# Kernel tuning notes

Measured on AMD Instinct MI355X. Metric: run time of the kernel, lower is better.

The kernel has to match this reference:

```python
import jax, jax.numpy as jnp
import numpy as np
from jax import lax

B, S, D, NH, K = 4, 2048, 1024, 16, 3
EPS = 1e-6


def custom_layernorm(x, gamma, beta):
    # torch-style: std with ddof=1, eps added to std (not var)
    mean = jnp.mean(x, axis=-1, keepdims=True)
    var = jnp.sum((x - mean) ** 2, axis=-1, keepdims=True) / (x.shape[-1] - 1)
    std = jnp.sqrt(var)
    return gamma * ((x - mean) / (std + EPS)) + beta


def setup_inputs() -> dict:
    key = jax.random.key(0)
    ks = jax.random.split(key, 10)
    s = 1.0 / np.sqrt(D)
    return {
        "x": jax.random.normal(ks[0], (B, S, D), jnp.float32),
        "Wq": jax.random.normal(ks[1], (D, D), jnp.float32) * s,
        "bq": jax.random.normal(ks[2], (D,), jnp.float32) * 0.02,
        "Wk": jax.random.normal(ks[3], (D, D), jnp.float32) * s,
        "Wv": jax.random.normal(ks[4], (D, D), jnp.float32) * s,
        "bv": jax.random.normal(ks[5], (D,), jnp.float32) * 0.02,
        "conv_w": jax.random.normal(ks[6], (D, D // NH, K), jnp.float32) * (1.0 / np.sqrt((D // NH) * K)),
        "conv_b": jax.random.normal(ks[7], (D,), jnp.float32) * 0.02,
        "gamma": jnp.ones((D,), jnp.float32),
        "beta": jnp.zeros((D,), jnp.float32),
        "Wo": jax.random.normal(ks[8], (D, D), jnp.float32) * s,
        "bo": jax.random.normal(ks[9], (D,), jnp.float32) * 0.02,
    }


def reference(x, Wq, bq, Wk, Wv, bv, conv_w, conv_b, gamma, beta, Wo, bo):
    d = x.shape[-1]
    groups = d // conv_w.shape[1]
    pad = conv_w.shape[2] // 2

    q = x @ Wq + bq
    k = x @ Wk  # key has no bias
    v = x @ Wv + bv

    # grouped conv1d over sequence dim (NCW layout)
    xc = jnp.transpose(x, (0, 2, 1))  # [B, D, S]
    conv_out = lax.conv_general_dilated(
        xc, conv_w, window_strides=(1,), padding=[(pad, pad)],
        feature_group_count=groups,
        dimension_numbers=("NCH", "OIH", "NCH"),
    ) + conv_b[None, :, None]
    conv_out = jnp.transpose(conv_out, (0, 2, 1))  # [B, S, D]
    conv_out = custom_layernorm(conv_out, gamma, beta)  # dropout = identity (eval)

    scale = 1.0 / jnp.sqrt(jnp.asarray(d, x.dtype))
    scores = jnp.einsum("bqd,bkd->bqk", q, k) * scale  # [B, S, S]
    attn = jax.nn.softmax(scores, axis=-1)
    attention_out = jnp.einsum("bqk,bkd->bqd", attn, v)

    combined = custom_layernorm(conv_out + attention_out, gamma, beta)
    return combined @ Wo + bo + x
```

## Files before the change

kernel.cpp:

```cpp
#include <hip/hip_runtime.h>
#include <cstdint>


#define DEV __device__ __forceinline__

typedef unsigned short u16;
typedef __attribute__((ext_vector_type(8))) short bf16x8;
typedef __attribute__((ext_vector_type(4))) float f32x4;

static const int Sn = 2048, Dn = 1024;

DEV float bf2f(u16 u) { union { unsigned int i; float f; } w; w.i = ((unsigned int)u) << 16; return w.f; }
DEV u16 f2bf(float f) {
  union { float f; unsigned int i; } w; w.f = f;
  unsigned int x = w.i;
  return (u16)((x + 0x7FFFu + ((x >> 16) & 1u)) >> 16);
}

DEV void gload_lds16(const u16* gsrc, u16* lds_dst) {
  __builtin_amdgcn_global_load_lds(
      (const __attribute__((address_space(1))) void*)gsrc,
      (__attribute__((address_space(3))) void*)lds_dst,
      16, 0, 0);
}

DEV float block_allreduce_sum(float v, float* red, int tid) {
  #pragma unroll
  for (int o = 32; o > 0; o >>= 1) v += __shfl_down(v, o, 64);
  __syncthreads();
  if ((tid & 63) == 0) red[tid >> 6] = v;
  __syncthreads();
  return red[0] + red[1] + red[2] + red[3];
}

DEV float block_allreduce_max(float v, float* red, int tid) {
  #pragma unroll
  for (int o = 32; o > 0; o >>= 1) v = fmaxf(v, __shfl_down(v, o, 64));
  __syncthreads();
  if ((tid & 63) == 0) red[tid >> 6] = v;
  __syncthreads();
  return fmaxf(fmaxf(red[0], red[1]), fmaxf(red[2], red[3]));
}

__global__ __launch_bounds__(256)
void prep_all(const float* __restrict__ Wq, const float* __restrict__ Wk,
              const float* __restrict__ Wv, const float* __restrict__ Wo,
              u16* __restrict__ wT,
              const float* __restrict__ bq, const float* __restrict__ bv,
              float* __restrict__ qkvb,
              const float* __restrict__ cw, u16* __restrict__ wconv,
              const float* __restrict__ x, u16* __restrict__ xb) {
  __shared__ u16 sm[64][68];
  int blk = blockIdx.x;
  int tid = threadIdx.x;
  if (blk < 1024) {
    int w = blk >> 8, t = blk & 255;
    const float* src = (w == 0) ? Wq : (w == 1) ? Wk : (w == 2) ? Wv : Wo;
    u16* dst = wT + (size_t)w * 1048576u;
    int i0 = (t >> 4) << 6, j0 = (t & 15) << 6;
    int tx = tid & 15, r0 = tid >> 4;
    #pragma unroll
    for (int rr = r0; rr < 64; rr += 16) {
      float4 v = *(const float4*)&src[(long)(i0 + rr) * 1024 + j0 + tx * 4];
      sm[rr][tx*4+0] = f2bf(v.x); sm[rr][tx*4+1] = f2bf(v.y);
      sm[rr][tx*4+2] = f2bf(v.z); sm[rr][tx*4+3] = f2bf(v.w);
    }
    __syncthreads();
    #pragma unroll
    for (int cc = r0; cc < 64; cc += 16) {
      ushort4 o;
      o.x = sm[tx*4+0][cc]; o.y = sm[tx*4+1][cc];
      o.z = sm[tx*4+2][cc]; o.w = sm[tx*4+3][cc];
      *(ushort4*)&dst[(long)(j0 + cc) * 1024 + i0 + tx * 4] = o;
    }
  } else if (blk < 1040) {
    int oc0 = (blk - 1024) * 64;
    for (int idx = tid; idx < 64 * 192; idx += 256) {
      int oc = oc0 + idx / 192; int k = idx % 192;
      int t = k >> 6, i = k & 63;
      wconv[(long)oc * 192 + k] = f2bf(cw[(long)oc * 192 + i * 3 + t]);
    }
  } else if (blk == 1040) {
    for (int j = tid; j < 3072; j += 256) {
      float v = 0.0f;
      if (j < 1024) v = bq[j];
      else if (j >= 2048) v = bv[j - 2048];
      qkvb[j] = v;
    }
  } else {
    int i = (blk - 1041) * 1024 + tid * 4;
    float4 v = *(const float4*)&x[i];
    ushort4 o;
    o.x = f2bf(v.x); o.y = f2bf(v.y); o.z = f2bf(v.z); o.w = f2bf(v.w);
    *(ushort4*)&xb[i] = o;
  }
}

template<typename CT>
__global__ __launch_bounds__(256, 2)
void gemm_nt(const u16* __restrict__ A, const u16* __restrict__ A2, long Abs, int lda,
             const u16* __restrict__ B, long Bbs, int ldb,
             CT* __restrict__ C, CT* __restrict__ C2, long Cbs, int ldc,
             int zsplit, int K, float scale,
             const float* __restrict__ bias, int bias_bs,
             const float* __restrict__ res, long Rbs, int ldr) {
  __shared__ u16 sA[2][128 * 32];
  __shared__ u16 sB[2][128 * 32];
  int tid = threadIdx.x;
  int lane = tid & 63, wv = tid >> 6;
  int quad = lane >> 4, lm = lane & 15;
  int wr = wv >> 1, wc = wv & 1;
  long m0 = (long)blockIdx.x * 128, n0 = (long)blockIdx.y * 128;
  int z = blockIdx.z;
  if (z >= zsplit) { A = A2 + (long)(z - zsplit) * Abs; C = C2 + (long)(z - zsplit) * Cbs; }
  else             { A = A  + (long)z * Abs;            C = C  + (long)z * Cbs; }
  B += (long)z * Bbs;
  if (res) res += (long)z * Rbs;

  f32x4 acc[4][4] = {};

  int srow = wv * 16 + (lane >> 2);
  int sch = (lane & 3) * 8;
  const u16* Ap = A + (m0 + srow) * (long)lda + sch;
  const u16* Bp = B + (n0 + srow) * (long)ldb + sch;
  const int lofs = wv * 16 * 32;

  for (int k0 = 0; k0 < K; k0 += 64) {
    #pragma unroll
    for (int h = 0; h < 2; h++) {
      int kh = k0 + h * 32;
      gload_lds16(Ap + kh, &sA[h][lofs]);
      gload_lds16(Ap + 64 * (long)lda + kh, &sA[h][lofs + 64 * 32]);
      gload_lds16(Bp + kh, &sB[h][lofs]);
      gload_lds16(Bp + 64 * (long)ldb + kh, &sB[h][lofs + 64 * 32]);
    }
    __syncthreads();
    #pragma unroll
    for (int h = 0; h < 2; h++) {
      bf16x8 af[4], bfr[4];
      #pragma unroll
      for (int mi = 0; mi < 4; mi++)
        af[mi] = *(const bf16x8*)&sA[h][(wr * 64 + mi * 16 + lm) * 32 + quad * 8];
      #pragma unroll
      for (int ni = 0; ni < 4; ni++)
        bfr[ni] = *(const bf16x8*)&sB[h][(wc * 64 + ni * 16 + lm) * 32 + quad * 8];
      #pragma unroll
      for (int mi = 0; mi < 4; mi++)
        #pragma unroll
        for (int ni = 0; ni < 4; ni++)
          acc[mi][ni] = __builtin_amdgcn_mfma_f32_16x16x32_bf16(af[mi], bfr[ni], acc[mi][ni], 0, 0, 0);
    }
    __syncthreads();
  }

  #pragma unroll
  for (int mi = 0; mi < 4; mi++) {
    #pragma unroll
    for (int ni = 0; ni < 4; ni++) {
      int col = (int)n0 + wc * 64 + ni * 16 + lm;
      float bv = bias ? bias[(long)z * bias_bs + col] : 0.0f;
      #pragma unroll
      for (int r = 0; r < 4; r++) {
        long rowg = m0 + wr * 64 + mi * 16 + quad * 4 + r;
        float v = acc[mi][ni][r] * scale + bv;
        if (res) v += res[rowg * (long)ldr + col];
        if constexpr (sizeof(CT) == 2) C[rowg * (long)ldc + col] = f2bf(v);
        else                           C[rowg * (long)ldc + col] = v;
      }
    }
  }
}

__global__ __launch_bounds__(256)
void mid_all(const u16* __restrict__ xb, const u16* __restrict__ wt,
             const float* __restrict__ cb, u16* __restrict__ convo,
             const u16* __restrict__ Vb, u16* __restrict__ vt) {
  __shared__ u16 smem[9360];
  int blk = blockIdx.x;
  int tid = threadIdx.x;
  if (blk < 1024) {
    u16 (*sx)[72] = (u16(*)[72])smem;
    int s0 = (blk & 15) * 128;
    int g = (blk >> 4) & 15;
    int b = blk >> 8;
    int lane = tid & 63, wv = tid >> 6;
    int quad = lane >> 4, lm = lane & 15;
    for (int idx = tid; idx < 130 * 16; idx += 256) {
      int r = idx >> 4, c4 = (idx & 15) * 4;
      int s = s0 - 1 + r;
      ushort4 v;
      if (s >= 0 && s < Sn) v = *(const ushort4*)&xb[((long)b * Sn + s) * Dn + g * 64 + c4];
      else { v.x = 0; v.y = 0; v.z = 0; v.w = 0; }
      *(ushort4*)&sx[r][c4] = v;
    }
    __syncthreads();
    f32x4 acc[2][4] = {};
    const u16* wg = wt + (long)g * 64 * 192;
    #pragma unroll
    for (int ks = 0; ks < 6; ks++) {
      int t = ks >> 1;
      int i0 = (ks & 1) * 32 + quad * 8;
      bf16x8 a0 = *(const bf16x8*)&sx[wv * 32 + lm + t][i0];
      bf16x8 a1 = *(const bf16x8*)&sx[wv * 32 + 16 + lm + t][i0];
      #pragma unroll
      for (int nf = 0; nf < 4; nf++) {
        bf16x8 bf = *(const bf16x8*)&wg[(nf * 16 + lm) * 192 + ks * 32 + quad * 8];
        acc[0][nf] = __builtin_amdgcn_mfma_f32_16x16x32_bf16(a0, bf, acc[0][nf], 0, 0, 0);
        acc[1][nf] = __builtin_amdgcn_mfma_f32_16x16x32_bf16(a1, bf, acc[1][nf], 0, 0, 0);
      }
    }
    #pragma unroll
    for (int mi = 0; mi < 2; mi++) {
      #pragma unroll
      for (int nf = 0; nf < 4; nf++) {
        int col = g * 64 + nf * 16 + lm;
        float bias = cb[col];
        #pragma unroll
        for (int r = 0; r < 4; r++) {
          int row = wv * 32 + mi * 16 + quad * 4 + r;
          convo[((long)b * Sn + s0 + row) * Dn + col] = f2bf(acc[mi][nf][r] + bias);
        }
      }
    }
  } else {
    u16 (*sm)[68] = (u16(*)[68])smem;
    int t = blk - 1024;
    int b = t >> 9, r = t & 511;
    int j0 = (r & 15) << 6, i0 = ((r >> 4) & 31) << 6;
    const u16* s = Vb + (long)b * Sn * Dn;
    u16* d = vt + (long)b * Dn * Sn;
    int tx = tid & 15, r0 = tid >> 4;
    #pragma unroll
    for (int rr = r0; rr < 64; rr += 16) {
      ushort4 v = *(const ushort4*)&s[(long)(i0 + rr) * 1024 + j0 + tx * 4];
      sm[rr][tx*4+0] = v.x; sm[rr][tx*4+1] = v.y; sm[rr][tx*4+2] = v.z; sm[rr][tx*4+3] = v.w;
    }
    __syncthreads();
    #pragma unroll
    for (int cc = r0; cc < 64; cc += 16) {
      ushort4 o;
      o.x = sm[tx*4+0][cc]; o.y = sm[tx*4+1][cc];
      o.z = sm[tx*4+2][cc]; o.w = sm[tx*4+3][cc];
      *(ushort4*)&d[(long)(j0 + cc) * 2048 + i0 + tx * 4] = o;
    }
  }
}

__global__ __launch_bounds__(256)
void ln_kernel(const u16* __restrict__ a, const u16* __restrict__ b2,
               const float* __restrict__ gamma, const float* __restrict__ beta,
               u16* __restrict__ out) {
  __shared__ float red[4];
  long row = blockIdx.x;
  int tid = threadIdx.x;
  long base = row * Dn + tid * 4;
  ushort4 av = *(const ushort4*)&a[base];
  float v0 = bf2f(av.x), v1 = bf2f(av.y), v2 = bf2f(av.z), v3 = bf2f(av.w);
  if (b2) {
    ushort4 bv4 = *(const ushort4*)&b2[base];
    v0 += bf2f(bv4.x); v1 += bf2f(bv4.y); v2 += bf2f(bv4.z); v3 += bf2f(bv4.w);
  }
  float s = block_allreduce_sum(v0 + v1 + v2 + v3, red, tid);
  float mean = s * (1.0f / 1024.0f);
  float d0 = v0 - mean, d1 = v1 - mean, d2 = v2 - mean, d3 = v3 - mean;
  float sq = block_allreduce_sum(d0 * d0 + d1 * d1 + d2 * d2 + d3 * d3, red, tid);
  float inv = 1.0f / (sqrtf(sq * (1.0f / 1023.0f)) + 1e-6f);
  float4 gv = *(const float4*)&gamma[tid * 4];
  float4 bev = *(const float4*)&beta[tid * 4];
  ushort4 o;
  o.x = f2bf(gv.x * d0 * inv + bev.x);
  o.y = f2bf(gv.y * d1 * inv + bev.y);
  o.z = f2bf(gv.z * d2 * inv + bev.z);
  o.w = f2bf(gv.w * d3 * inv + bev.w);
  *(ushort4*)&out[base] = o;
}

__global__ __launch_bounds__(256)
void softmax_bf16(u16* __restrict__ pa, u16* __restrict__ pb, int rowsplit) {
  __shared__ float red[4];
  long row = blockIdx.x;
  u16* p = (row < rowsplit) ? pa + row * 2048 : pb + (row - rowsplit) * 2048;
  int tid = threadIdx.x;
  ushort4 a = *(const ushort4*)&p[tid * 8];
  ushort4 b = *(const ushort4*)&p[tid * 8 + 4];
  float f0 = bf2f(a.x), f1 = bf2f(a.y), f2 = bf2f(a.z), f3 = bf2f(a.w);
  float f4 = bf2f(b.x), f5 = bf2f(b.y), f6 = bf2f(b.z), f7 = bf2f(b.w);
  float m = fmaxf(fmaxf(fmaxf(f0, f1), fmaxf(f2, f3)),
                  fmaxf(fmaxf(f4, f5), fmaxf(f6, f7)));
  m = block_allreduce_max(m, red, tid);
  float e0 = __expf(f0 - m), e1 = __expf(f1 - m), e2 = __expf(f2 - m), e3 = __expf(f3 - m);
  float e4 = __expf(f4 - m), e5 = __expf(f5 - m), e6 = __expf(f6 - m), e7 = __expf(f7 - m);
  float s = block_allreduce_sum(e0 + e1 + e2 + e3 + e4 + e5 + e6 + e7, red, tid);
  float inv = 1.0f / s;
  ushort4 o1, o2;
  o1.x = f2bf(e0 * inv); o1.y = f2bf(e1 * inv); o1.z = f2bf(e2 * inv); o1.w = f2bf(e3 * inv);
  o2.x = f2bf(e4 * inv); o2.y = f2bf(e5 * inv); o2.z = f2bf(e6 * inv); o2.w = f2bf(e7 * inv);
  *(ushort4*)&p[tid * 8] = o1;
  *(ushort4*)&p[tid * 8 + 4] = o2;
}

static const size_t OFF_WT    = 0;
static const size_t OFF_QKVB  = 8ull << 20;
static const size_t OFF_WCONV = (8ull << 20) + (64 << 10);
static const size_t OFF_Q     = 9ull << 20;
static const size_t OFF_K     = 25ull << 20;
static const size_t OFF_V     = 41ull << 20;
static const size_t OFF_PW    = 57ull << 20;

extern "C" void kernel_launch(void* const* d_in, const int* in_sizes, int n_in,
                              void* d_out, int out_size, void* d_ws, size_t ws_size,
                              hipStream_t stream) {
  const float* x     = (const float*)d_in[0];
  const float* Wq    = (const float*)d_in[1];
  const float* bq    = (const float*)d_in[2];
  const float* Wk    = (const float*)d_in[3];
  const float* Wv    = (const float*)d_in[4];
  const float* bv    = (const float*)d_in[5];
  const float* cw    = (const float*)d_in[6];
  const float* cb    = (const float*)d_in[7];
  const float* gamma = (const float*)d_in[8];
  const float* beta  = (const float*)d_in[9];
  const float* Wo    = (const float*)d_in[10];
  const float* bo    = (const float*)d_in[11];
  float* out = (float*)d_out;
  char* ws = (char*)d_ws;

  u16*   wT    = (u16*)(ws + OFF_WT);
  float* qkvb  = (float*)(ws + OFF_QKVB);
  u16*   wconv = (u16*)(ws + OFF_WCONV);
  u16*   Qb    = (u16*)(ws + OFF_Q);
  u16*   Kb    = (u16*)(ws + OFF_K);
  u16*   Vb    = (u16*)(ws + OFF_V);
  u16*   Pw    = (u16*)(ws + OFF_PW);
  u16*   xb    = (u16*)d_out;
  u16*   Pd    = (u16*)d_out;
  u16*   vt    = (u16*)d_out + 8388608;
  u16*   conv  = Vb;
  u16*   attn  = Qb;
  u16*   combined = Kb;
  const long PBS = (long)Sn * Sn;

  dim3 tb(256);

  prep_all<<<dim3(9233), tb, 0, stream>>>(Wq, Wk, Wv, Wo, wT, bq, bv, qkvb,
                                          cw, wconv, x, xb);
  gemm_nt<u16><<<dim3(64, 8, 3), tb, 0, stream>>>(
      xb, nullptr, 0, 1024, wT, 1048576, 1024, Qb, (u16*)nullptr, 8388608, 1024,
      99, 1024, 1.0f, qkvb, 1024, nullptr, 0, 0);
  mid_all<<<dim3(3072), tb, 0, stream>>>(xb, wconv, cb, conv, Vb, vt);
  ln_kernel<<<dim3(8192), tb, 0, stream>>>(conv, nullptr, gamma, beta, conv);

  if (ws_size >= (73ull << 20)) {
    gemm_nt<u16><<<dim3(16, 16, 4), tb, 0, stream>>>(
        Qb, Qb + 2 * (long)Sn * Dn, (long)Sn * Dn, 1024,
        Kb, (long)Sn * Dn, 1024,
        Pd, Pw, PBS, 2048,
        2, 1024, 0.03125f, nullptr, 0, nullptr, 0, 0);
    softmax_bf16<<<dim3(8192), tb, 0, stream>>>(Pd, Pw, 4096);
    gemm_nt<u16><<<dim3(16, 8, 4), tb, 0, stream>>>(
        Pd, Pw, PBS, 2048,
        vt, (long)Dn * Sn, 2048,
        attn, attn + 2 * (long)Sn * Dn, (long)Sn * Dn, 1024,
        2, 2048, 1.0f, nullptr, 0, nullptr, 0, 0);
  } else {
    for (int c = 0; c < 2; c++) {
      long off = (long)c * 2 * Sn * Dn;
      gemm_nt<u16><<<dim3(16, 16, 2), tb, 0, stream>>>(
          Qb + off, nullptr, (long)Sn * Dn, 1024, Kb + off, (long)Sn * Dn, 1024,
          Pd, (u16*)nullptr, PBS, 2048,
          99, 1024, 0.03125f, nullptr, 0, nullptr, 0, 0);
      softmax_bf16<<<dim3(4096), tb, 0, stream>>>(Pd, Pd, 4096);
      gemm_nt<u16><<<dim3(16, 8, 2), tb, 0, stream>>>(
          Pd, nullptr, PBS, 2048, vt + off, (long)Dn * Sn, 2048,
          attn + off, (u16*)nullptr, (long)Sn * Dn, 1024,
          99, 2048, 1.0f, nullptr, 0, nullptr, 0, 0);
    }
  }

  ln_kernel<<<dim3(8192), tb, 0, stream>>>(conv, attn, gamma, beta, combined);
  gemm_nt<float><<<dim3(64, 8, 1), tb, 0, stream>>>(
      combined, nullptr, 0, 1024, wT + 3u * 1048576u, 0, 1024,
      out, (float*)nullptr, 0, 1024,
      99, 1024, 1.0f, bo, 0, x, 0, 1024);
}
```

Before: 359.4 us.

## Co-schedule independent conv, transpose and LN work inside attention GEMM and softmax kernels

Restructures the cross-stage schedule by packing independent work into the same launches. The V transpose now runs as extra blocks beside the QK^T GEMM, the grouped conv (weights converted in-block from fp32, input read from fp32 x) beside softmax, and the conv LayerNorm beside the PV GEMM. This cuts two kernel launches and the serial gaps between them, and lets the small kernels fill idle CUs during the GEMM tail. The cost is an inlined GEMM without the general kernel's pipelining parameters, more shared memory for the softmax blocks, and conv blocks that redo the weight conversion per group.

```diff
diff --git a/kernel.cpp b/kernel.cpp
--- a/kernel.cpp
+++ b/kernel.cpp
@@ -42,13 +42,37 @@
   return fmaxf(fmaxf(red[0], red[1]), fmaxf(red[2], red[3]));
 }
 
+DEV void ln_row(const u16* __restrict__ a, const u16* __restrict__ b2,
+                const float* __restrict__ gamma, const float* __restrict__ beta,
+                u16* __restrict__ out, long row, int tid, float* red) {
+  long base = row * Dn + tid * 4;
+  ushort4 av = *(const ushort4*)&a[base];
+  float v0 = bf2f(av.x), v1 = bf2f(av.y), v2 = bf2f(av.z), v3 = bf2f(av.w);
+  if (b2) {
+    ushort4 bv4 = *(const ushort4*)&b2[base];
+    v0 += bf2f(bv4.x); v1 += bf2f(bv4.y); v2 += bf2f(bv4.z); v3 += bf2f(bv4.w);
+  }
+  float s = block_allreduce_sum(v0 + v1 + v2 + v3, red, tid);
+  float mean = s * (1.0f / 1024.0f);
+  float d0 = v0 - mean, d1 = v1 - mean, d2 = v2 - mean, d3 = v3 - mean;
+  float sq = block_allreduce_sum(d0 * d0 + d1 * d1 + d2 * d2 + d3 * d3, red, tid);
+  float inv = 1.0f / (sqrtf(sq * (1.0f / 1023.0f)) + 1e-6f);
+  float4 gv = *(const float4*)&gamma[tid * 4];
+  float4 bev = *(const float4*)&beta[tid * 4];
+  ushort4 o;
+  o.x = f2bf(gv.x * d0 * inv + bev.x);
+  o.y = f2bf(gv.y * d1 * inv + bev.y);
+  o.z = f2bf(gv.z * d2 * inv + bev.z);
+  o.w = f2bf(gv.w * d3 * inv + bev.w);
+  *(ushort4*)&out[base] = o;
+}
+
 __global__ __launch_bounds__(256)
 void prep_all(const float* __restrict__ Wq, const float* __restrict__ Wk,
               const float* __restrict__ Wv, const float* __restrict__ Wo,
               u16* __restrict__ wT,
               const float* __restrict__ bq, const float* __restrict__ bv,
               float* __restrict__ qkvb,
-              const float* __restrict__ cw, u16* __restrict__ wconv,
               const float* __restrict__ x, u16* __restrict__ xb) {
   __shared__ u16 sm[64][68];
   int blk = blockIdx.x;
@@ -73,14 +97,7 @@
       o.z = sm[tx*4+2][cc]; o.w = sm[tx*4+3][cc];
       *(ushort4*)&dst[(long)(j0 + cc) * 1024 + i0 + tx * 4] = o;
     }
-  } else if (blk < 1040) {
-    int oc0 = (blk - 1024) * 64;
-    for (int idx = tid; idx < 64 * 192; idx += 256) {
-      int oc = oc0 + idx / 192; int k = idx % 192;
-      int t = k >> 6, i = k & 63;
-      wconv[(long)oc * 192 + k] = f2bf(cw[(long)oc * 192 + i * 3 + t]);
-    }
-  } else if (blk == 1040) {
+  } else if (blk == 1024) {
     for (int j = tid; j < 3072; j += 256) {
       float v = 0.0f;
       if (j < 1024) v = bq[j];
@@ -88,7 +105,7 @@
       qkvb[j] = v;
     }
   } else {
-    int i = (blk - 1041) * 1024 + tid * 4;
+    int i = (blk - 1025) * 1024 + tid * 4;
     float4 v = *(const float4*)&x[i];
     ushort4 o;
     o.x = f2bf(v.x); o.y = f2bf(v.y); o.z = f2bf(v.z); o.w = f2bf(v.w);
@@ -171,31 +188,149 @@
   }
 }
 
-__global__ __launch_bounds__(256)
-void mid_all(const u16* __restrict__ xb, const u16* __restrict__ wt,
-             const float* __restrict__ cb, u16* __restrict__ convo,
-             const u16* __restrict__ Vb, u16* __restrict__ vt) {
-  __shared__ u16 smem[9360];
+__global__ __launch_bounds__(256, 2)
+void post_qkv(int ngemm,
+              const u16* __restrict__ Qb, const u16* __restrict__ Kb,
+              u16* __restrict__ Pd, u16* __restrict__ Pw,
+              const u16* __restrict__ Vb, u16* __restrict__ vt) {
+  __shared__ u16 smem[2 * 2 * 128 * 32];
   int blk = blockIdx.x;
   int tid = threadIdx.x;
-  if (blk < 1024) {
-    u16 (*sx)[72] = (u16(*)[72])smem;
-    int s0 = (blk & 15) * 128;
-    int g = (blk >> 4) & 15;
-    int b = blk >> 8;
+  if (blk < ngemm) {
+    u16* sA0 = smem;
+    u16* sB0 = smem + 2 * 128 * 32;
     int lane = tid & 63, wv = tid >> 6;
     int quad = lane >> 4, lm = lane & 15;
+    int wr = wv >> 1, wc = wv & 1;
+    int z = blk >> 8;
+    long m0 = (long)(blk & 15) * 128, n0 = (long)((blk >> 4) & 15) * 128;
+    const u16* A = Qb + (long)z * Sn * Dn;
+    const u16* B = Kb + (long)z * Sn * Dn;
+    u16* C = (z < 2) ? Pd + (long)z * Sn * Sn : Pw + (long)(z - 2) * Sn * Sn;
+
+    f32x4 acc[4][4] = {};
+    int srow = wv * 16 + (lane >> 2);
+    int sch = (lane & 3) * 8;
+    const u16* Ap = A + (m0 + srow) * 1024 + sch;
+    const u16* Bp = B + (n0 + srow) * 1024 + sch;
+    const int lofs = wv * 16 * 32;
+
+    for (int k0 = 0; k0 < 1024; k0 += 64) {
+      #pragma unroll
+      for (int h = 0; h < 2; h++) {
+        int kh = k0 + h * 32;
+        gload_lds16(Ap + kh, &sA0[h * 128 * 32 + lofs]);
+        gload_lds16(Ap + 64 * 1024 + kh, &sA0[h * 128 * 32 + lofs + 64 * 32]);
+        gload_lds16(Bp + kh, &sB0[h * 128 * 32 + lofs]);
+        gload_lds16(Bp + 64 * 1024 + kh, &sB0[h * 128 * 32 + lofs + 64 * 32]);
+      }
+      __syncthreads();
+      #pragma unroll
+      for (int h = 0; h < 2; h++) {
+        bf16x8 af[4], bfr[4];
+        #pragma unroll
+        for (int mi = 0; mi < 4; mi++)
+          af[mi] = *(const bf16x8*)&sA0[h * 128 * 32 + (wr * 64 + mi * 16 + lm) * 32 + quad * 8];
+        #pragma unroll
+        for (int ni = 0; ni < 4; ni++)
+          bfr[ni] = *(const bf16x8*)&sB0[h * 128 * 32 + (wc * 64 + ni * 16 + lm) * 32 + quad * 8];
+        #pragma unroll
+        for (int mi = 0; mi < 4; mi++)
+          #pragma unroll
+          for (int ni = 0; ni < 4; ni++)
+            acc[mi][ni] = __builtin_amdgcn_mfma_f32_16x16x32_bf16(af[mi], bfr[ni], acc[mi][ni], 0, 0, 0);
+      }
+      __syncthreads();
+    }
+    #pragma unroll
+    for (int mi = 0; mi < 4; mi++) {
+      #pragma unroll
+      for (int ni = 0; ni < 4; ni++) {
+        int col = (int)n0 + wc * 64 + ni * 16 + lm;
+        #pragma unroll
+        for (int r = 0; r < 4; r++) {
+          long rowg = m0 + wr * 64 + mi * 16 + quad * 4 + r;
+          C[rowg * 2048 + col] = f2bf(acc[mi][ni][r] * 0.03125f);
+        }
+      }
+    }
+  } else {
+    u16 (*sm)[68] = (u16(*)[68])smem;
+    int t = blk - ngemm;
+    int b = t >> 9, r = t & 511;
+    int j0 = (r & 15) << 6, i0 = ((r >> 4) & 31) << 6;
+    const u16* s = Vb + (long)b * Sn * Dn;
+    u16* d = vt + (long)b * Dn * Sn;
+    int tx = tid & 15, r0 = tid >> 4;
+    #pragma unroll
+    for (int rr = r0; rr < 64; rr += 16) {
+      ushort4 v = *(const ushort4*)&s[(long)(i0 + rr) * 1024 + j0 + tx * 4];
+      sm[rr][tx*4+0] = v.x; sm[rr][tx*4+1] = v.y; sm[rr][tx*4+2] = v.z; sm[rr][tx*4+3] = v.w;
+    }
+    __syncthreads();
+    #pragma unroll
+    for (int cc = r0; cc < 64; cc += 16) {
+      ushort4 o;
+      o.x = sm[tx*4+0][cc]; o.y = sm[tx*4+1][cc];
+      o.z = sm[tx*4+2][cc]; o.w = sm[tx*4+3][cc];
+      *(ushort4*)&d[(long)(j0 + cc) * 2048 + i0 + tx * 4] = o;
+    }
+  }
+}
+
+__global__ __launch_bounds__(256)
+void smax_conv(u16* __restrict__ pa, u16* __restrict__ pb, int rowsplit, int nsm,
+               const float* __restrict__ x, const float* __restrict__ cw,
+               const float* __restrict__ cb, u16* __restrict__ convo) {
+  __shared__ u16 smem[22160];
+  __shared__ float red[4];
+  int blk = blockIdx.x;
+  int tid = threadIdx.x;
+  if (blk < nsm) {
+    long row = blk;
+    u16* p = (row < rowsplit) ? pa + row * 2048 : pb + (row - rowsplit) * 2048;
+    ushort4 a = *(const ushort4*)&p[tid * 8];
+    ushort4 b = *(const ushort4*)&p[tid * 8 + 4];
+    float f0 = bf2f(a.x), f1 = bf2f(a.y), f2 = bf2f(a.z), f3 = bf2f(a.w);
+    float f4 = bf2f(b.x), f5 = bf2f(b.y), f6 = bf2f(b.z), f7 = bf2f(b.w);
+    float m = fmaxf(fmaxf(fmaxf(f0, f1), fmaxf(f2, f3)),
+                    fmaxf(fmaxf(f4, f5), fmaxf(f6, f7)));
+    m = block_allreduce_max(m, red, tid);
+    float e0 = __expf(f0 - m), e1 = __expf(f1 - m), e2 = __expf(f2 - m), e3 = __expf(f3 - m);
+    float e4 = __expf(f4 - m), e5 = __expf(f5 - m), e6 = __expf(f6 - m), e7 = __expf(f7 - m);
+    float s = block_allreduce_sum(e0 + e1 + e2 + e3 + e4 + e5 + e6 + e7, red, tid);
+    float inv = 1.0f / s;
+    ushort4 o1, o2;
+    o1.x = f2bf(e0 * inv); o1.y = f2bf(e1 * inv); o1.z = f2bf(e2 * inv); o1.w = f2bf(e3 * inv);
+    o2.x = f2bf(e4 * inv); o2.y = f2bf(e5 * inv); o2.z = f2bf(e6 * inv); o2.w = f2bf(e7 * inv);
+    *(ushort4*)&p[tid * 8] = o1;
+    *(ushort4*)&p[tid * 8 + 4] = o2;
+  } else {
+    u16 (*sx)[72] = (u16(*)[72])smem;
+    u16 (*sw)[200] = (u16(*)[200])(smem + 9360);
+    int r = blk - nsm;
+    int s0 = (r & 15) * 128;
+    int g = (r >> 4) & 15;
+    int b = r >> 8;
+    int lane = tid & 63, wv = tid >> 6;
+    int quad = lane >> 4, lm = lane & 15;
+    for (int idx = tid; idx < 64 * 192; idx += 256) {
+      int oc = idx / 192, k = idx - oc * 192;
+      int t = k >> 6, i = k & 63;
+      sw[oc][k] = f2bf(cw[((long)(g * 64 + oc)) * 192 + i * 3 + t]);
+    }
     for (int idx = tid; idx < 130 * 16; idx += 256) {
-      int r = idx >> 4, c4 = (idx & 15) * 4;
-      int s = s0 - 1 + r;
+      int rr = idx >> 4, c4 = (idx & 15) * 4;
+      int s = s0 - 1 + rr;
       ushort4 v;
-      if (s >= 0 && s < Sn) v = *(const ushort4*)&xb[((long)b * Sn + s) * Dn + g * 64 + c4];
-      else { v.x = 0; v.y = 0; v.z = 0; v.w = 0; }
-      *(ushort4*)&sx[r][c4] = v;
+      if (s >= 0 && s < Sn) {
+        float4 f = *(const float4*)&x[((long)b * Sn + s) * Dn + g * 64 + c4];
+        v.x = f2bf(f.x); v.y = f2bf(f.y); v.z = f2bf(f.z); v.w = f2bf(f.w);
+      } else { v.x = 0; v.y = 0; v.z = 0; v.w = 0; }
+      *(ushort4*)&sx[rr][c4] = v;
     }
     __syncthreads();
     f32x4 acc[2][4] = {};
-    const u16* wg = wt + (long)g * 64 * 192;
     #pragma unroll
     for (int ks = 0; ks < 6; ks++) {
       int t = ks >> 1;
@@ -204,7 +339,7 @@
       bf16x8 a1 = *(const bf16x8*)&sx[wv * 32 + 16 + lm + t][i0];
       #pragma unroll
       for (int nf = 0; nf < 4; nf++) {
-        bf16x8 bf = *(const bf16x8*)&wg[(nf * 16 + lm) * 192 + ks * 32 + quad * 8];
+        bf16x8 bf = *(const bf16x8*)&sw[nf * 16 + lm][ks * 32 + quad * 8];
         acc[0][nf] = __builtin_amdgcn_mfma_f32_16x16x32_bf16(a0, bf, acc[0][nf], 0, 0, 0);
         acc[1][nf] = __builtin_amdgcn_mfma_f32_16x16x32_bf16(a1, bf, acc[1][nf], 0, 0, 0);
       }
@@ -216,33 +351,86 @@
         int col = g * 64 + nf * 16 + lm;
         float bias = cb[col];
         #pragma unroll
+        for (int rr = 0; rr < 4; rr++) {
+          int row = wv * 32 + mi * 16 + quad * 4 + rr;
+          convo[((long)b * Sn + s0 + row) * Dn + col] = f2bf(acc[mi][nf][rr] + bias);
+        }
+      }
+    }
+  }
+}
+
+__global__ __launch_bounds__(256, 2)
+void pv_ln(int npv,
+           const u16* __restrict__ Pd, const u16* __restrict__ Pw,
+           const u16* __restrict__ vt, u16* __restrict__ attn,
+           u16* __restrict__ conv,
+           const float* __restrict__ gamma, const float* __restrict__ beta) {
+  __shared__ u16 smem[2 * 2 * 128 * 32];
+  __shared__ float red[4];
+  int blk = blockIdx.x;
+  int tid = threadIdx.x;
+  if (blk < npv) {
+    u16* sA0 = smem;
+    u16* sB0 = smem + 2 * 128 * 32;
+    int lane = tid & 63, wv = tid >> 6;
+    int quad = lane >> 4, lm = lane & 15;
+    int wr = wv >> 1, wc = wv & 1;
+    int z = blk >> 7;
+    long m0 = (long)(blk & 15) * 128, n0 = (long)((blk >> 4) & 7) * 128;
+    const u16* A = (z < 2) ? Pd + (long)z * Sn * Sn : Pw + (long)(z - 2) * Sn * Sn;
+    const u16* B = vt + (long)z * Dn * Sn;
+    u16* C = attn + (long)z * Sn * Dn;
+
+    f32x4 acc[4][4] = {};
+    int srow = wv * 16 + (lane >> 2);
+    int sch = (lane & 3) * 8;
+    const u16* Ap = A + (m0 + srow) * 2048 + sch;
+    const u16* Bp = B + (n0 + srow) * 2048 + sch;
+    const int lofs = wv * 16 * 32;
+
+    for (int k0 = 0; k0 < 2048; k0 += 64) {
+      #pragma unroll
+      for (int h = 0; h < 2; h++) {
+        int kh = k0 + h * 32;
+        gload_lds16(Ap + kh, &sA0[h * 128 * 32 + lofs]);
+        gload_lds16(Ap + 64 * 2048 + kh, &sA0[h * 128 * 32 + lofs + 64 * 32]);
+        gload_lds16(Bp + kh, &sB0[h * 128 * 32 + lofs]);
+        gload_lds16(Bp + 64 * 2048 + kh, &sB0[h * 128 * 32 + lofs + 64 * 32]);
+      }
+      __syncthreads();
+      #pragma unroll
+      for (int h = 0; h < 2; h++) {
+        bf16x8 af[4], bfr[4];
+        #pragma unroll
+        for (int mi = 0; mi < 4; mi++)
+          af[mi] = *(const bf16x8*)&sA0[h * 128 * 32 + (wr * 64 + mi * 16 + lm) * 32 + quad * 8];
+        #pragma unroll
+        for (int ni = 0; ni < 4; ni++)
+          bfr[ni] = *(const bf16x8*)&sB0[h * 128 * 32 + (wc * 64 + ni * 16 + lm) * 32 + quad * 8];
+        #pragma unroll
+        for (int mi = 0; mi < 4; mi++)
+          #pragma unroll
+          for (int ni = 0; ni < 4; ni++)
+            acc[mi][ni] = __builtin_amdgcn_mfma_f32_16x16x32_bf16(af[mi], bfr[ni], acc[mi][ni], 0, 0, 0);
+      }
+      __syncthreads();
+    }
+    #pragma unroll
+    for (int mi = 0; mi < 4; mi++) {
+      #pragma unroll
+      for (int ni = 0; ni < 4; ni++) {
+        int col = (int)n0 + wc * 64 + ni * 16 + lm;
+        #pragma unroll
         for (int r = 0; r < 4; r++) {
-          int row = wv * 32 + mi * 16 + quad * 4 + r;
-          convo[((long)b * Sn + s0 + row) * Dn + col] = f2bf(acc[mi][nf][r] + bias);
+          long rowg = m0 + wr * 64 + mi * 16 + quad * 4 + r;
+          C[rowg * 1024 + col] = f2bf(acc[mi][ni][r]);
         }
       }
     }
   } else {
-    u16 (*sm)[68] = (u16(*)[68])smem;
-    int t = blk - 1024;
-    int b = t >> 9, r = t & 511;
-    int j0 = (r & 15) << 6, i0 = ((r >> 4) & 31) << 6;
-    const u16* s = Vb + (long)b * Sn * Dn;
-    u16* d = vt + (long)b * Dn * Sn;
-    int tx = tid & 15, r0 = tid >> 4;
-    #pragma unroll
-    for (int rr = r0; rr < 64; rr += 16) {
-      ushort4 v = *(const ushort4*)&s[(long)(i0 + rr) * 1024 + j0 + tx * 4];
-      sm[rr][tx*4+0] = v.x; sm[rr][tx*4+1] = v.y; sm[rr][tx*4+2] = v.z; sm[rr][tx*4+3] = v.w;
-    }
-    __syncthreads();
-    #pragma unroll
-    for (int cc = r0; cc < 64; cc += 16) {
-      ushort4 o;
-      o.x = sm[tx*4+0][cc]; o.y = sm[tx*4+1][cc];
-      o.z = sm[tx*4+2][cc]; o.w = sm[tx*4+3][cc];
-      *(ushort4*)&d[(long)(j0 + cc) * 2048 + i0 + tx * 4] = o;
-    }
+    long row = blk - npv;
+    ln_row(conv, nullptr, gamma, beta, conv, row, tid, red);
   }
 }
 
@@ -251,57 +439,11 @@
                const float* __restrict__ gamma, const float* __restrict__ beta,
                u16* __restrict__ out) {
   __shared__ float red[4];
-  long row = blockIdx.x;
-  int tid = threadIdx.x;
-  long base = row * Dn + tid * 4;
-  ushort4 av = *(const ushort4*)&a[base];
-  float v0 = bf2f(av.x), v1 = bf2f(av.y), v2 = bf2f(av.z), v3 = bf2f(av.w);
-  if (b2) {
-    ushort4 bv4 = *(const ushort4*)&b2[base];
-    v0 += bf2f(bv4.x); v1 += bf2f(bv4.y); v2 += bf2f(bv4.z); v3 += bf2f(bv4.w);
-  }
-  float s = block_allreduce_sum(v0 + v1 + v2 + v3, red, tid);
-  float mean = s * (1.0f / 1024.0f);
-  float d0 = v0 - mean, d1 = v1 - mean, d2 = v2 - mean, d3 = v3 - mean;
-  float sq = block_allreduce_sum(d0 * d0 + d1 * d1 + d2 * d2 + d3 * d3, red, tid);
-  float inv = 1.0f / (sqrtf(sq * (1.0f / 1023.0f)) + 1e-6f);
-  float4 gv = *(const float4*)&gamma[tid * 4];
-  float4 bev = *(const float4*)&beta[tid * 4];
-  ushort4 o;
-  o.x = f2bf(gv.x * d0 * inv + bev.x);
-  o.y = f2bf(gv.y * d1 * inv + bev.y);
-  o.z = f2bf(gv.z * d2 * inv + bev.z);
-  o.w = f2bf(gv.w * d3 * inv + bev.w);
-  *(ushort4*)&out[base] = o;
-}
-
-__global__ __launch_bounds__(256)
-void softmax_bf16(u16* __restrict__ pa, u16* __restrict__ pb, int rowsplit) {
-  __shared__ float red[4];
-  long row = blockIdx.x;
-  u16* p = (row < rowsplit) ? pa + row * 2048 : pb + (row - rowsplit) * 2048;
-  int tid = threadIdx.x;
-  ushort4 a = *(const ushort4*)&p[tid * 8];
-  ushort4 b = *(const ushort4*)&p[tid * 8 + 4];
-  float f0 = bf2f(a.x), f1 = bf2f(a.y), f2 = bf2f(a.z), f3 = bf2f(a.w);
-  float f4 = bf2f(b.x), f5 = bf2f(b.y), f6 = bf2f(b.z), f7 = bf2f(b.w);
-  float m = fmaxf(fmaxf(fmaxf(f0, f1), fmaxf(f2, f3)),
-                  fmaxf(fmaxf(f4, f5), fmaxf(f6, f7)));
-  m = block_allreduce_max(m, red, tid);
-  float e0 = __expf(f0 - m), e1 = __expf(f1 - m), e2 = __expf(f2 - m), e3 = __expf(f3 - m);
-  float e4 = __expf(f4 - m), e5 = __expf(f5 - m), e6 = __expf(f6 - m), e7 = __expf(f7 - m);
-  float s = block_allreduce_sum(e0 + e1 + e2 + e3 + e4 + e5 + e6 + e7, red, tid);
-  float inv = 1.0f / s;
-  ushort4 o1, o2;
-  o1.x = f2bf(e0 * inv); o1.y = f2bf(e1 * inv); o1.z = f2bf(e2 * inv); o1.w = f2bf(e3 * inv);
-  o2.x = f2bf(e4 * inv); o2.y = f2bf(e5 * inv); o2.z = f2bf(e6 * inv); o2.w = f2bf(e7 * inv);
-  *(ushort4*)&p[tid * 8] = o1;
-  *(ushort4*)&p[tid * 8 + 4] = o2;
+  ln_row(a, b2, gamma, beta, out, blockIdx.x, threadIdx.x, red);
 }
 
 static const size_t OFF_WT    = 0;
 static const size_t OFF_QKVB  = 8ull << 20;
-static const size_t OFF_WCONV = (8ull << 20) + (64 << 10);
 static const size_t OFF_Q     = 9ull << 20;
 static const size_t OFF_K     = 25ull << 20;
 static const size_t OFF_V     = 41ull << 20;
@@ -327,7 +469,6 @@
 
   u16*   wT    = (u16*)(ws + OFF_WT);
   float* qkvb  = (float*)(ws + OFF_QKVB);
-  u16*   wconv = (u16*)(ws + OFF_WCONV);
   u16*   Qb    = (u16*)(ws + OFF_Q);
   u16*   Kb    = (u16*)(ws + OFF_K);
   u16*   Vb    = (u16*)(ws + OFF_V);
@@ -342,39 +483,33 @@
 
   dim3 tb(256);
 
-  prep_all<<<dim3(9233), tb, 0, stream>>>(Wq, Wk, Wv, Wo, wT, bq, bv, qkvb,
-                                          cw, wconv, x, xb);
+  prep_all<<<dim3(9217), tb, 0, stream>>>(Wq, Wk, Wv, Wo, wT, bq, bv, qkvb, x, xb);
   gemm_nt<u16><<<dim3(64, 8, 3), tb, 0, stream>>>(
       xb, nullptr, 0, 1024, wT, 1048576, 1024, Qb, (u16*)nullptr, 8388608, 1024,
       99, 1024, 1.0f, qkvb, 1024, nullptr, 0, 0);
-  mid_all<<<dim3(3072), tb, 0, stream>>>(xb, wconv, cb, conv, Vb, vt);
-  ln_kernel<<<dim3(8192), tb, 0, stream>>>(conv, nullptr, gamma, beta, conv);
 
   if (ws_size >= (73ull << 20)) {
-    gemm_nt<u16><<<dim3(16, 16, 4), tb, 0, stream>>>(
-        Qb, Qb + 2 * (long)Sn * Dn, (long)Sn * Dn, 1024,
-        Kb, (long)Sn * Dn, 1024,
-        Pd, Pw, PBS, 2048,
-        2, 1024, 0.03125f, nullptr, 0, nullptr, 0, 0);
-    softmax_bf16<<<dim3(8192), tb, 0, stream>>>(Pd, Pw, 4096);
-    gemm_nt<u16><<<dim3(16, 8, 4), tb, 0, stream>>>(
-        Pd, Pw, PBS, 2048,
-        vt, (long)Dn * Sn, 2048,
-        attn, attn + 2 * (long)Sn * Dn, (long)Sn * Dn, 1024,
-        2, 2048, 1.0f, nullptr, 0, nullptr, 0, 0);
+    post_qkv<<<dim3(1024 + 2048), tb, 0, stream>>>(1024, Qb, Kb, Pd, Pw, Vb, vt);
+    smax_conv<<<dim3(8192 + 1024), tb, 0, stream>>>(Pd, Pw, 4096, 8192,
+                                                    x, cw, cb, conv);
+    pv_ln<<<dim3(512 + 8192), tb, 0, stream>>>(512, Pd, Pw, vt, attn, conv,
+                                               gamma, beta);
   } else {
+    post_qkv<<<dim3(2048), tb, 0, stream>>>(0, Qb, Kb, Pd, Pw, Vb, vt);
     for (int c = 0; c < 2; c++) {
       long off = (long)c * 2 * Sn * Dn;
       gemm_nt<u16><<<dim3(16, 16, 2), tb, 0, stream>>>(
           Qb + off, nullptr, (long)Sn * Dn, 1024, Kb + off, (long)Sn * Dn, 1024,
           Pd, (u16*)nullptr, PBS, 2048,
           99, 1024, 0.03125f, nullptr, 0, nullptr, 0, 0);
-      softmax_bf16<<<dim3(4096), tb, 0, stream>>>(Pd, Pd, 4096);
+      smax_conv<<<dim3(4096 + (c == 0 ? 1024 : 0)), tb, 0, stream>>>(
+          Pd, Pd, 4096, 4096, x, cw, cb, conv);
       gemm_nt<u16><<<dim3(16, 8, 2), tb, 0, stream>>>(
           Pd, nullptr, PBS, 2048, vt + off, (long)Dn * Sn, 2048,
           attn + off, (u16*)nullptr, (long)Sn * Dn, 1024,
           99, 2048, 1.0f, nullptr, 0, nullptr, 0, 0);
     }
+    ln_kernel<<<dim3(8192), tb, 0, stream>>>(conv, nullptr, gamma, beta, conv);
   }
 
   ln_kernel<<<dim3(8192), tb, 0, stream>>>(conv, attn, gamma, beta, combined);
```

Measured after the change: 355.8 us (median of 2 runs). No clear change (-1.0%).
